# Optimization experiments

Hardware: AMD Instinct MI355X
Metric: run time of the kernel (lower is better)

## Reference

```python
import jax, jax.numpy as jnp
import numpy as np

B, D, H, DR, DM = 16384, 384, 1024, 512, 1152
KP, KN = 3, 2
K = KP + KN
RG_C = 8.0

def setup_inputs() -> dict:
    key = jax.random.key(0)
    ks = jax.random.split(key, 24)
    def n(k, shape, scale=1.0):
        return jax.random.normal(k, shape, jnp.float32) * scale
    s = lambda fan: 1.0 / np.sqrt(fan).astype(np.float32)
    return dict(
        init_f=n(ks[0], (B, D)),
        head_embs=n(ks[1], (K, B, D)),
        pred_embs=n(ks[2], (K, B, D)),
        w_ap=n(ks[3], (D, 1), s(D)), b_ap=jnp.zeros((1,), jnp.float32),
        w_an=n(ks[4], (D, 1), s(D)), b_an=jnp.zeros((1,), jnp.float32),
        nt_w1=n(ks[5], (D, H), s(D)), nt_b1=jnp.zeros((H,), jnp.float32),
        nt_w2=n(ks[6], (H, D), s(H)), nt_b2=jnp.zeros((D,), jnp.float32),
        g1=jnp.ones((D,), jnp.float32),
        rg_wx=n(ks[7], (D, DR), s(D)), rg_bx=jnp.zeros((DR,), jnp.float32),
        rg_wy=n(ks[8], (D, DR), s(D)), rg_by=jnp.zeros((DR,), jnp.float32),
        rg_wr=n(ks[9], (DR, DR), s(DR)), rg_br=jnp.zeros((DR,), jnp.float32),
        rg_wi=n(ks[10], (DR, DR), s(DR)), rg_bi=jnp.zeros((DR,), jnp.float32),
        rg_lam=n(ks[11], (DR,), 0.5),
        rg_wo=n(ks[12], (DR, D), s(DR)), rg_bo=jnp.zeros((D,), jnp.float32),
        g2=jnp.ones((D,), jnp.float32),
        mlp_wg=n(ks[13], (D, DM), s(D)),
        mlp_wv=n(ks[14], (D, DM), s(D)),
        mlp_wo=n(ks[15], (DM, D), s(DM)),
        fa_wg=n(ks[16], (D, D), s(D)),
        fa_wv=n(ks[17], (D, D), s(D)),
        fa_wo=n(ks[18], (D, D), s(D)),
        fa_wl=n(ks[19], (D, 1), s(D)), fa_bl=jnp.zeros((1,), jnp.float32),
    )

def rmsnorm(x, g, eps=1e-6):
    return x * g * jax.lax.rsqrt(jnp.mean(x * x, axis=-1, keepdims=True) + eps)

def rg_lru(x, wr, br, wi, bi, lam):
    # x: [B, S, DR] -> gated linear recurrence over S (Griffin RG-LRU)
    a_base = -RG_C * jax.nn.softplus(lam)  # [DR]
    def step(h, xt):
        r = jax.nn.sigmoid(xt @ wr + br)
        i = jax.nn.sigmoid(xt @ wi + bi)
        log_a = a_base * r
        h = jnp.exp(log_a) * h + jnp.sqrt(1.0 - jnp.exp(2.0 * log_a)) * (i * xt)
        return h, h
    h0 = jnp.zeros((x.shape[0], x.shape[2]), x.dtype)
    _, ys = jax.lax.scan(step, h0, jnp.swapaxes(x, 0, 1))
    return jnp.swapaxes(ys, 0, 1)

def reference(init_f, head_embs, pred_embs, w_ap, b_ap, w_an, b_an,
              nt_w1, nt_b1, nt_w2, nt_b2, g1,
              rg_wx, rg_bx, rg_wy, rg_by, rg_wr, rg_br, rg_wi, rg_bi,
              rg_lam, rg_wo, rg_bo, g2, mlp_wg, mlp_wv, mlp_wo,
              fa_wg, fa_wv, fa_wo, fa_wl, fa_bl):
    # message passing: estimate_tail_emb(head, pred) = head + pred (TransE-style)
    msg = head_embs + pred_embs                       # [K, B, D]
    pos = jnp.transpose(msg[:KP], (1, 0, 2))          # [B, KP, D]
    neg = jnp.transpose(msg[KP:], (1, 0, 2))          # [B, KN, D]
    # signed residual for negated atomics: -m + MLP(m)
    neg = -neg + jax.nn.relu(neg @ nt_w1 + nt_b1) @ nt_w2 + nt_b2
    # grouped softmax attention over the positive / negative message lists
    aw_p = jax.nn.softmax(pos @ w_ap + b_ap, axis=1)  # [B, KP, 1]
    aw_n = jax.nn.softmax(neg @ w_an + b_an, axis=1)  # [B, KN, 1]
    x = jnp.concatenate([init_f[:, None, :], pos * aw_p, neg * aw_n], axis=1)  # [B, S=6, D]
    # Griffin block (depth=1): recurrent residual branch
    h = rmsnorm(x, g1)
    u = h @ rg_wx + rg_bx                             # [B, S, DR]
    y = rg_lru(u, rg_wr, rg_br, rg_wi, rg_bi, rg_lam)
    gate = jax.nn.gelu(h @ rg_wy + rg_by)
    x = x + (y * gate) @ rg_wo + rg_bo
    # gated-MLP residual branch
    h2 = rmsnorm(x, g2)
    x = x + (jax.nn.gelu(h2 @ mlp_wg) * (h2 @ mlp_wv)) @ mlp_wo
    # final attention aggregation: Gated_MLP_block -> Linear(D,1) -> softmax -> mean
    fa = (jax.nn.gelu(x @ fa_wg) * (x @ fa_wv)) @ fa_wo
    w = jax.nn.softmax(fa @ fa_wl + fa_bl, axis=1)    # [B, S, 1]
    return jnp.mean(x * w, axis=1)                    # [B, D], agg_func='mean'
```

## Files before the change

kernel.cpp:

```cpp
#include <hip/hip_runtime.h>
#include <hip/hip_bf16.h>

#define B_TOT 16384
#define DD    384
#define HH    1024
#define DRR   512
#define DMM   1152
#define SS    6
#define KPP   3
#define KNN   2

typedef unsigned short ushort_t;
typedef __bf16 bf16x8 __attribute__((ext_vector_type(8)));
typedef float  f32x4  __attribute__((ext_vector_type(4)));

#define CST 136
#define EPW 72

__device__ __forceinline__ float fexp2(float x) { return __builtin_amdgcn_exp2f(x); }
__device__ __forceinline__ float frcp(float x)  { return __builtin_amdgcn_rcpf(x); }
__device__ __forceinline__ float sigmoid_f(float x) {
    return frcp(1.f + fexp2(-1.4426950408889634f * x));
}
__device__ __forceinline__ float gelu_f(float x) {
    float z = 0.7978845608028654f * x * (1.f + 0.044715f * x * x);
    return x * frcp(1.f + fexp2(-2.885390081777927f * z));
}
__device__ __forceinline__ float wave_red_sum(float v) {
    #pragma unroll
    for (int off = 32; off; off >>= 1) v += __shfl_xor(v, off);
    return v;
}
__device__ __forceinline__ ushort_t f2bf(float v) {
    __hip_bfloat16 h = __float2bfloat16(v);
    return *reinterpret_cast<ushort_t*>(&h);
}
__device__ __forceinline__ float bf2f(ushort_t u) {
    unsigned int x = ((unsigned int)u) << 16;
    return __uint_as_float(x);
}
__device__ __forceinline__ void g2l16(const ushort_t* g, ushort_t* l) {
    __builtin_amdgcn_global_load_lds(
        (const __attribute__((address_space(1))) void*)g,
        (__attribute__((address_space(3))) void*)l, 16, 0, 0);
}
__device__ __forceinline__ void swz_xy(int& bx, int& by) {
    const int nx = gridDim.x;
    const int nwg = nx * gridDim.y;
    const int h = by * nx + bx;
    const int q = nwg >> 3, r = nwg & 7;
    const int xcd = h & 7, lo = h >> 3;
    const int lin = (xcd < r) ? (xcd * (q + 1) + lo)
                              : (r * (q + 1) + (xcd - r) * q + lo);
    bx = lin % nx;
    by = lin / nx;
}

template<int EPI, bool ACCUM>
__global__ __launch_bounds__(256, 2)
void bgemm(const ushort_t* __restrict__ A, const ushort_t* __restrict__ WT,
           const float* __restrict__ bias, const ushort_t* __restrict__ X2,
           float* __restrict__ C, ushort_t* __restrict__ Ch, ushort_t* __restrict__ Ch2,
           int M, int N, int K)
{
    __shared__ ushort_t sm[32768];

    int bx = blockIdx.x, by = blockIdx.y;
    swz_xy(bx, by);
    const int tid = threadIdx.x;
    const int l = tid & 63, w = tid >> 6;
    const int wr = w >> 1, wc = w & 1;
    const int lr = l & 15, hi = l >> 4;
    const int row0 = by * 128, col0 = bx * 128;

    const int lrw = l >> 3;
    const int lch = (l & 7) ^ (lrw & 7);
    const ushort_t* As[4]; const ushort_t* Bs[4]; int lo_[4];
    #pragma unroll
    for (int i = 0; i < 4; ++i) {
        const int g = w * 4 + i;
        As[i] = A  + (size_t)(row0 + g*8 + lrw) * K + lch * 8;
        Bs[i] = WT + (size_t)(col0 + g*8 + lrw) * K + lch * 8;
        lo_[i] = g * 512;
    }
    const int ko[2] = {(hi*8) ^ ((lr&7)*8), (32 + hi*8) ^ ((lr&7)*8)};

    f32x4 acc[4][4] = {};
    const int NT = K >> 6;

    #pragma unroll
    for (int i = 0; i < 4; ++i) {
        g2l16(As[i], &sm[lo_[i]]);
        g2l16(Bs[i], &sm[16384 + lo_[i]]);
    }
    __syncthreads();

    int db = 0;
    for (int t = 0; t < NT; ++t) {
        if (t + 1 < NT) {
            const int nb = db ^ 1;
            #pragma unroll
            for (int i = 0; i < 4; ++i) {
                g2l16(As[i] + (size_t)(t+1)*64, &sm[nb*8192 + lo_[i]]);
                g2l16(Bs[i] + (size_t)(t+1)*64, &sm[16384 + nb*8192 + lo_[i]]);
            }
        }
        #pragma unroll
        for (int ks = 0; ks < 2; ++ks) {
            bf16x8 af[4], bfr[4];
            #pragma unroll
            for (int m = 0; m < 4; ++m)
                af[m] = *(const bf16x8*)&sm[db*8192 + (wr*64 + m*16 + lr)*64 + ko[ks]];
            #pragma unroll
            for (int n = 0; n < 4; ++n)
                bfr[n] = *(const bf16x8*)&sm[16384 + db*8192 + (wc*64 + n*16 + lr)*64 + ko[ks]];
            #pragma unroll
            for (int m = 0; m < 4; ++m)
                #pragma unroll
                for (int n = 0; n < 4; ++n)
                    acc[m][n] = __builtin_amdgcn_mfma_f32_16x16x32_bf16(
                        af[m], bfr[n], acc[m][n], 0, 0, 0);
        }
        __syncthreads();
        db ^= 1;
    }

    const bool BF = (EPI == 7) || (Ch != nullptr);
    #pragma unroll
    for (int m = 0; m < 4; ++m) {
        #pragma unroll
        for (int n = 0; n < 4; ++n) {
            const int r0 = row0 + wr*64 + m*16 + hi*4;
            const int c  = col0 + wc*64 + n*16 + lr;
            const float bv = bias ? bias[c] : 0.f;
            #pragma unroll
            for (int j = 0; j < 4; ++j) {
                const int r = r0 + j;
                float v = acc[m][n][j] + bv;
                if (EPI == 1) v = fmaxf(v, 0.f);
                if (EPI == 4) v = v - bf2f(X2[(size_t)r * N + c]);
                if (ACCUM)    v += C[(size_t)r * N + c];
                if (C) C[(size_t)r * N + c] = v;
                if (BF) {
                    float ov = (EPI == 7 && c >= 512) ? gelu_f(v) : v;
                    sm[(wr*64 + m*16 + hi*4 + j) * CST + wc*64 + n*16 + lr] = f2bf(ov);
                }
            }
        }
    }
    if (BF) {
        __syncthreads();
        const int er = tid >> 1, ec = (tid & 1) * 64;
        ushort_t* dst; int nn, dc0;
        if (EPI == 7) {
            nn = 512;
            if (col0 < 512) { dst = Ch;  dc0 = col0; }
            else            { dst = Ch2; dc0 = col0 - 512; }
        } else { dst = Ch; nn = N; dc0 = col0; }
        const uint4* sp = (const uint4*)&sm[er * CST + ec];
        uint4* gp = (uint4*)(dst + (size_t)(row0 + er) * nn + dc0 + ec);
        #pragma unroll
        for (int q = 0; q < 8; ++q) gp[q] = sp[q];
    }
}

template<bool LOGITS>
__global__ __launch_bounds__(256, 2)
void dual_k(const ushort_t* __restrict__ A, const ushort_t* __restrict__ W1T,
            const ushort_t* __restrict__ W2T, ushort_t* __restrict__ Ch,
            float* __restrict__ LP, const float* __restrict__ wproj,
            int M, int N, int K)
{
    __shared__ ushort_t sm[32768];

    int bx = blockIdx.x, by = blockIdx.y;
    swz_xy(bx, by);
    const int tid = threadIdx.x;
    const int l = tid & 63, w = tid >> 6;
    const int wr = w >> 1, wc = w & 1;
    const int lr = l & 15, hi = l >> 4;
    const int row0 = by * 128, col0 = bx * 64;

    const int lrw = l >> 3;
    const int lch = (l & 7) ^ (lrw & 7);
    const ushort_t* As[4]; int loA[4];
    #pragma unroll
    for (int i = 0; i < 4; ++i) {
        const int g = w * 4 + i;
        As[i] = A + (size_t)(row0 + g*8 + lrw) * K + lch * 8;
        loA[i] = g * 512;
    }
    const ushort_t* Gs[2]; const ushort_t* Vs[2]; int loB[2];
    #pragma unroll
    for (int i = 0; i < 2; ++i) {
        const int g = w * 2 + i;
        Gs[i] = W1T + (size_t)(col0 + g*8 + lrw) * K + lch * 8;
        Vs[i] = W2T + (size_t)(col0 + g*8 + lrw) * K + lch * 8;
        loB[i] = g * 512;
    }
    const int ko[2] = {(hi*8) ^ ((lr&7)*8), (32 + hi*8) ^ ((lr&7)*8)};

    f32x4 ag[4][2] = {}, av[4][2] = {};
    const int NT = K >> 6;

    #pragma unroll
    for (int i = 0; i < 4; ++i) g2l16(As[i], &sm[loA[i]]);
    #pragma unroll
    for (int i = 0; i < 2; ++i) {
        g2l16(Gs[i], &sm[16384 + loB[i]]);
        g2l16(Vs[i], &sm[24576 + loB[i]]);
    }
    __syncthreads();

    int db = 0;
    for (int t = 0; t < NT; ++t) {
        if (t + 1 < NT) {
            const int nb = db ^ 1;
            #pragma unroll
            for (int i = 0; i < 4; ++i)
                g2l16(As[i] + (size_t)(t+1)*64, &sm[nb*8192 + loA[i]]);
            #pragma unroll
            for (int i = 0; i < 2; ++i) {
                g2l16(Gs[i] + (size_t)(t+1)*64, &sm[16384 + nb*4096 + loB[i]]);
                g2l16(Vs[i] + (size_t)(t+1)*64, &sm[24576 + nb*4096 + loB[i]]);
            }
        }
        #pragma unroll
        for (int ks = 0; ks < 2; ++ks) {
            bf16x8 af[4], bg[2], bv[2];
            #pragma unroll
            for (int m = 0; m < 4; ++m)
                af[m] = *(const bf16x8*)&sm[db*8192 + (wr*64 + m*16 + lr)*64 + ko[ks]];
            #pragma unroll
            for (int n = 0; n < 2; ++n) {
                bg[n] = *(const bf16x8*)&sm[16384 + db*4096 + (wc*32 + n*16 + lr)*64 + ko[ks]];
                bv[n] = *(const bf16x8*)&sm[24576 + db*4096 + (wc*32 + n*16 + lr)*64 + ko[ks]];
            }
            #pragma unroll
            for (int m = 0; m < 4; ++m)
                #pragma unroll
                for (int n = 0; n < 2; ++n) {
                    ag[m][n] = __builtin_amdgcn_mfma_f32_16x16x32_bf16(af[m], bg[n], ag[m][n], 0, 0, 0);
                    av[m][n] = __builtin_amdgcn_mfma_f32_16x16x32_bf16(af[m], bv[n], av[m][n], 0, 0, 0);
                }
        }
        __syncthreads();
        db ^= 1;
    }

    if (!LOGITS) {
        #pragma unroll
        for (int m = 0; m < 4; ++m)
            #pragma unroll
            for (int n = 0; n < 2; ++n)
                #pragma unroll
                for (int j = 0; j < 4; ++j)
                    sm[(wr*64 + m*16 + hi*4 + j) * EPW + wc*32 + n*16 + lr] =
                        f2bf(gelu_f(ag[m][n][j]) * av[m][n][j]);
        __syncthreads();
        const int er = tid >> 1, ec = (tid & 1) * 32;
        const uint4* sp = (const uint4*)&sm[er * EPW + ec];
        uint4* gp = (uint4*)(Ch + (size_t)(row0 + er) * N + col0 + ec);
        #pragma unroll
        for (int q = 0; q < 4; ++q) gp[q] = sp[q];
    } else {
        float wp[2];
        #pragma unroll
        for (int n = 0; n < 2; ++n) wp[n] = wproj[col0 + wc*32 + n*16 + lr];
        float* red = (float*)sm;
        #pragma unroll
        for (int m = 0; m < 4; ++m) {
            #pragma unroll
            for (int j = 0; j < 4; ++j) {
                float s = 0.f;
                #pragma unroll
                for (int n = 0; n < 2; ++n)
                    s += gelu_f(ag[m][n][j]) * av[m][n][j] * wp[n];
                s += __shfl_xor(s, 1);
                s += __shfl_xor(s, 2);
                s += __shfl_xor(s, 4);
                s += __shfl_xor(s, 8);
                if (lr == 0) red[(wr*64 + m*16 + hi*4 + j) * 2 + wc] = s;
            }
        }
        __syncthreads();
        if (tid < 128)
            LP[(size_t)(row0 + tid) * 6 + bx] = red[tid*2] + red[tid*2 + 1];
    }
}

__global__ __launch_bounds__(256, 8)
void rec_k(ushort_t* __restrict__ u, const ushort_t* __restrict__ gate,
           const ushort_t* __restrict__ ri, const float* __restrict__ a2,
           int Bc)
{
    const int g = blockIdx.x * 256 + threadIdx.x;
    const int b = g >> 6, c8 = (g & 63) << 3;
    float a2v[8];
    *(float4*)&a2v[0] = *(const float4*)&a2[c8];
    *(float4*)&a2v[4] = *(const float4*)&a2[c8 + 4];
    float h[8] = {};
    for (int t = 0; t < SS; ++t) {
        const size_t row = (size_t)t * Bc + b;
        uint4 uw = *(const uint4*)&u[row * DRR + c8];
        uint4 rw = *(const uint4*)&ri[row * 1024 + c8];
        uint4 iw = *(const uint4*)&ri[row * 1024 + 512 + c8];
        uint4 gw = *(const uint4*)&gate[row * DRR + c8];
        const ushort_t* up = (const ushort_t*)&uw;
        const ushort_t* rp = (const ushort_t*)&rw;
        const ushort_t* ip = (const ushort_t*)&iw;
        const ushort_t* gp = (const ushort_t*)&gw;
        ushort_t o[8];
        #pragma unroll
        for (int q = 0; q < 8; ++q) {
            const float rv = sigmoid_f(bf2f(rp[q]));
            const float iv = sigmoid_f(bf2f(ip[q]));
            const float e  = fexp2(a2v[q] * rv);
            const float hv = e * h[q]
                           + sqrtf(fmaxf(0.f, 1.f - e * e)) * (iv * bf2f(up[q]));
            h[q] = hv;
            o[q] = f2bf(hv * bf2f(gp[q]));
        }
        *(uint4*)&u[row * DRR + c8] = *(const uint4*)o;
    }
}


struct TrArgs { const float* W[12]; };
__global__ void tr_all_k(TrArgs a, ushort_t* __restrict__ wt)
{
    constexpr int KT[12]  = {384,1024,384,384,512,512,512,384,384,1152,384,384};
    constexpr int NTb[12] = {1024,384,512,512,512,512,384,1152,1152,384,384,384};
    constexpr int EOFF[12]= {0,393216,786432,983040,1179648,1441792,1703936,
                             1900544,2342912,2785280,3227648,3375104};
    constexpr int TPRE[13]= {0,384,768,960,1152,1408,1664,1856,2288,2720,3152,3296,3440};
    const int tb = blockIdx.x;
    int s = 0;
    #pragma unroll
    for (int i = 0; i < 12; ++i) if (tb >= TPRE[i+1]) s = i + 1;
    const int rel = tb - TPRE[s];
    const int K = KT[s], N = NTb[s];
    const int ntn = N >> 5;
    const int k0 = (rel / ntn) * 32, n0 = (rel % ntn) * 32;

    __shared__ float ts[32][33];
    const int r = threadIdx.x >> 3, c4 = (threadIdx.x & 7) * 4;
    const float4 v = *(const float4*)&a.W[s][(size_t)(k0 + r) * N + n0 + c4];
    ts[r][c4+0] = v.x; ts[r][c4+1] = v.y; ts[r][c4+2] = v.z; ts[r][c4+3] = v.w;
    __syncthreads();
    ushort_t o4[4];
    #pragma unroll
    for (int q = 0; q < 4; ++q) o4[q] = f2bf(ts[c4 + q][r]);
    *(uint2*)&wt[EOFF[s] + (size_t)(n0 + r) * K + k0 + c4] = *(const uint2*)o4;
}

__global__ void prep_k(const float* __restrict__ rg_bx, const float* __restrict__ rg_by,
                       const float* __restrict__ rg_lam,
                       const float* __restrict__ rg_br, const float* __restrict__ rg_bi,
                       float* __restrict__ bias_xy, float* __restrict__ a2,
                       float* __restrict__ bias_ri)
{
    int i = blockIdx.x * 256 + threadIdx.x;
    if (i < 512) {
        bias_xy[i] = rg_bx[i];
        bias_ri[i] = rg_br[i];
        float lam = rg_lam[i];
        float sp = (lam > 20.f) ? lam : log1pf(expf(lam));
        a2[i] = -8.0f * sp * 1.4426950408889634f;
    } else if (i < 1024) {
        bias_xy[i] = rg_by[i - 512];
        bias_ri[i] = rg_bi[i - 512];
    }
}

__global__ void negm_k(const float* __restrict__ head, const float* __restrict__ pred,
                       ushort_t* __restrict__ negm_h, int b0, int Bc)
{
    int idx = blockIdx.x * 256 + threadIdx.x;
    int d = idx % DD, rr = idx / DD;
    int j = (rr >= Bc) ? 1 : 0;
    int b = rr - j * Bc;
    size_t off = ((size_t)(KPP + j) * B_TOT + (b0 + b)) * DD + d;
    negm_h[idx] = f2bf(head[off] + pred[off]);
}

__global__ void asmrms_k(const float* __restrict__ init_f,
                         const float* __restrict__ head, const float* __restrict__ pred,
                         const float* __restrict__ w_ap, const float* __restrict__ b_ap,
                         const float* __restrict__ w_an, const float* __restrict__ b_an,
                         const ushort_t* __restrict__ nf, const float* __restrict__ g1,
                         float* __restrict__ x, ushort_t* __restrict__ hb,
                         int b0, int Bc)
{
    const int lb = blockIdx.x, gb = b0 + lb, lane = threadIdx.x;
    float hp[3][6], nv[2][6], iv[6], wap[6], wan[6];
    #pragma unroll
    for (int q = 0; q < 6; ++q) {
        int d = lane + 64 * q;
        wap[q] = w_ap[d]; wan[q] = w_an[d];
        iv[q] = init_f[(size_t)gb * DD + d];
    }
    float lp[3], ln2[2];
    #pragma unroll
    for (int j = 0; j < 3; ++j) {
        float p = 0.f;
        #pragma unroll
        for (int q = 0; q < 6; ++q) {
            int d = lane + 64 * q;
            size_t off = ((size_t)j * B_TOT + gb) * DD + d;
            float v = head[off] + pred[off];
            hp[j][q] = v;
            p += v * wap[q];
        }
        lp[j] = wave_red_sum(p) + b_ap[0];
    }
    #pragma unroll
    for (int j = 0; j < 2; ++j) {
        float p = 0.f;
        #pragma unroll
        for (int q = 0; q < 6; ++q) {
            int d = lane + 64 * q;
            float v = bf2f(nf[((size_t)j * Bc + lb) * DD + d]);
            nv[j][q] = v;
            p += v * wan[q];
        }
        ln2[j] = wave_red_sum(p) + b_an[0];
    }
    float mp = fmaxf(lp[0], fmaxf(lp[1], lp[2]));
    float e0 = expf(lp[0]-mp), e1 = expf(lp[1]-mp), e2 = expf(lp[2]-mp);
    float sp = e0 + e1 + e2;
    float awp[3] = {e0/sp, e1/sp, e2/sp};
    float mn = fmaxf(ln2[0], ln2[1]);
    float f0 = expf(ln2[0]-mn), f1 = expf(ln2[1]-mn);
    float sn = f0 + f1;
    float awn[2] = {f0/sn, f1/sn};

    #pragma unroll
    for (int t = 0; t < SS; ++t) {
        float rowv[6], ss = 0.f;
        #pragma unroll
        for (int q = 0; q < 6; ++q) {
            float v;
            if (t == 0)      v = iv[q];
            else if (t <= 3) v = hp[t-1][q] * awp[t-1];
            else             v = nv[t-4][q] * awn[t-4];
            rowv[q] = v;
            ss += v * v;
        }
        ss = wave_red_sum(ss);
        float sc = rsqrtf(ss / (float)DD + 1e-6f);
        float* xr = x + (size_t)(t * Bc + lb) * DD;
        ushort_t* hr = hb + (size_t)(t * Bc + lb) * DD;
        #pragma unroll
        for (int q = 0; q < 6; ++q) {
            int d = lane + 64 * q;
            xr[d] = rowv[q];
            hr[d] = f2bf(rowv[q] * g1[d] * sc);
        }
    }
}

__global__ void rms_k(const float* __restrict__ x, const float* __restrict__ g,
                      ushort_t* __restrict__ h)
{
    int row  = blockIdx.x * 4 + (threadIdx.x >> 6);
    int lane = threadIdx.x & 63;
    const float* xr = x + (size_t)row * DD;
    float ss = 0.f;
    for (int d = lane; d < DD; d += 64) { float v = xr[d]; ss += v * v; }
    ss = wave_red_sum(ss);
    float sc = rsqrtf(ss / (float)DD + 1e-6f);
    ushort_t* hr = h + (size_t)row * DD;
    for (int d = lane; d < DD; d += 64) hr[d] = f2bf(xr[d] * g[d] * sc);
}

__global__ void wproj_k(const float* __restrict__ fa_wo, const float* __restrict__ fa_wl,
                        float* __restrict__ wproj)
{
    int d = threadIdx.x;
    float s = 0.f;
    for (int k = 0; k < DD; ++k) s += fa_wo[(size_t)d * DD + k] * fa_wl[k];
    wproj[d] = s;
}

__global__ void final_k(const float* __restrict__ x, const float* __restrict__ lp,
                        const float* __restrict__ fa_bl,
                        float* __restrict__ out, int b0, int Bc)
{
    const int lb = blockIdx.x, gb = b0 + lb, lane = threadIdx.x;
    float lg[SS];
    #pragma unroll
    for (int t = 0; t < SS; ++t) {
        const float* pp = lp + (size_t)(t * Bc + lb) * 6;
        lg[t] = pp[0] + pp[1] + pp[2] + pp[3] + pp[4] + pp[5] + fa_bl[0];
    }
    float m = lg[0];
    #pragma unroll
    for (int t = 1; t < SS; ++t) m = fmaxf(m, lg[t]);
    float e[SS], s = 0.f;
    #pragma unroll
    for (int t = 0; t < SS; ++t) { e[t] = expf(lg[t] - m); s += e[t]; }
    float inv = 1.0f / s;
    #pragma unroll
    for (int q = 0; q < 6; ++q) {
        int d = lane + 64 * q;
        float acc = 0.f;
        #pragma unroll
        for (int t = 0; t < SS; ++t)
            acc += x[(size_t)(t * Bc + lb) * DD + d] * (e[t] * inv);
        out[(size_t)gb * DD + d] = acc * (1.0f / 6.0f);
    }
}

extern "C" void kernel_launch(void* const* d_in, const int* in_sizes, int n_in,
                              void* d_out, int out_size, void* d_ws, size_t ws_size,
                              hipStream_t stream)
{
    (void)in_sizes; (void)n_in; (void)out_size;
    const float* init_f  = (const float*)d_in[0];
    const float* head    = (const float*)d_in[1];
    const float* pred    = (const float*)d_in[2];
    const float* w_ap    = (const float*)d_in[3];
    const float* b_ap    = (const float*)d_in[4];
    const float* w_an    = (const float*)d_in[5];
    const float* b_an    = (const float*)d_in[6];
    const float* nt_w1   = (const float*)d_in[7];
    const float* nt_b1   = (const float*)d_in[8];
    const float* nt_w2   = (const float*)d_in[9];
    const float* nt_b2   = (const float*)d_in[10];
    const float* g1      = (const float*)d_in[11];
    const float* rg_wx   = (const float*)d_in[12];
    const float* rg_bx   = (const float*)d_in[13];
    const float* rg_wy   = (const float*)d_in[14];
    const float* rg_by   = (const float*)d_in[15];
    const float* rg_wr   = (const float*)d_in[16];
    const float* rg_br   = (const float*)d_in[17];
    const float* rg_wi   = (const float*)d_in[18];
    const float* rg_bi   = (const float*)d_in[19];
    const float* rg_lam  = (const float*)d_in[20];
    const float* rg_wo   = (const float*)d_in[21];
    const float* rg_bo   = (const float*)d_in[22];
    const float* g2      = (const float*)d_in[23];
    const float* mlp_wg  = (const float*)d_in[24];
    const float* mlp_wv  = (const float*)d_in[25];
    const float* mlp_wo  = (const float*)d_in[26];
    const float* fa_wg   = (const float*)d_in[27];
    const float* fa_wv   = (const float*)d_in[28];
    const float* fa_wo   = (const float*)d_in[29];
    const float* fa_wl   = (const float*)d_in[30];
    const float* fa_bl   = (const float*)d_in[31];
    float* out = (float*)d_out;

    float* ws_f    = (float*)d_ws;
    float* wproj   = ws_f;
    float* bias_xy = ws_f + 512;
    float* a2      = ws_f + 1536;
    float* bias_ri = ws_f + 2048;
    ushort_t* wt   = (ushort_t*)(ws_f + 3072);

    ushort_t* ntw1T = wt + 0;
    ushort_t* ntw2T = wt + 393216;
    ushort_t* wxyT  = wt + 786432;
    ushort_t* wriT  = wt + 1179648;
    ushort_t* woT   = wt + 1703936;
    ushort_t* mwgT  = wt + 1900544;
    ushort_t* mwvT  = wt + 2342912;
    ushort_t* mwoT  = wt + 2785280;
    ushort_t* fwgT  = wt + 3227648;
    ushort_t* fwvT  = wt + 3375104;

    TrArgs ta;
    ta.W[0]=nt_w1; ta.W[1]=nt_w2; ta.W[2]=rg_wx; ta.W[3]=rg_wy;
    ta.W[4]=rg_wr; ta.W[5]=rg_wi; ta.W[6]=rg_wo; ta.W[7]=mlp_wg;
    ta.W[8]=mlp_wv; ta.W[9]=mlp_wo; ta.W[10]=fa_wg; ta.W[11]=fa_wv;
    tr_all_k<<<3440, 256, 0, stream>>>(ta, wt);
    prep_k<<<4, 256, 0, stream>>>(rg_bx, rg_by, rg_lam, rg_br, rg_bi,
                                  bias_xy, a2, bias_ri);
    wproj_k<<<1, DD, 0, stream>>>(fa_wo, fa_wl, wproj);

    const size_t fixed_f32 = 3072 + 1761280;
    const size_t per_b_f32 = 8448;
    int Bc = B_TOT;
    while (Bc > 128 && (fixed_f32 + per_b_f32 * (size_t)Bc) * 4 > ws_size) Bc >>= 1;

    float* arena = ws_f + fixed_f32;

    for (int b0 = 0; b0 < B_TOT; b0 += Bc) {
        const int M  = Bc * SS;
        const int M2 = Bc * KNN;
        float*    xbuf = arena;
        ushort_t* negm = (ushort_t*)(arena + (size_t)2304 * Bc);
        ushort_t* hid  = (ushort_t*)(arena + (size_t)2688 * Bc);
        ushort_t* nf   = (ushort_t*)(arena + (size_t)3712 * Bc);
        ushort_t* hb   = (ushort_t*)(arena + (size_t)4096 * Bc);
        ushort_t* uh   = (ushort_t*)(arena + (size_t)5376 * Bc);
        ushort_t* gth  = (ushort_t*)(arena + (size_t)6912 * Bc);
        ushort_t* ri   = (ushort_t*)(arena + (size_t)2304 * Bc);
        ushort_t* h2   = (ushort_t*)(arena + (size_t)2304 * Bc);
        ushort_t* Th   = (ushort_t*)(arena + (size_t)3456 * Bc);
        ushort_t* xh   = (ushort_t*)(arena + (size_t)6912 * Bc);
        float*    lpb  = arena + (size_t)2304 * Bc;

        negm_k<<<Bc * 3, 256, 0, stream>>>(head, pred, negm, b0, Bc);
        bgemm<1, false><<<dim3(HH/128, M2/128), 256, 0, stream>>>(
            negm, ntw1T, nt_b1, nullptr, nullptr, hid, nullptr, M2, HH, DD);
        bgemm<4, false><<<dim3(DD/128, M2/128), 256, 0, stream>>>(
            hid, ntw2T, nt_b2, negm, nullptr, nf, nullptr, M2, DD, HH);
        asmrms_k<<<Bc, 64, 0, stream>>>(init_f, head, pred, w_ap, b_ap, w_an, b_an,
                                        nf, g1, xbuf, hb, b0, Bc);

        bgemm<7, false><<<dim3(1024/128, M/128), 256, 0, stream>>>(
            hb, wxyT, bias_xy, nullptr, nullptr, uh, gth, M, 1024, DD);
        bgemm<0, false><<<dim3(1024/128, M/128), 256, 0, stream>>>(
            uh, wriT, bias_ri, nullptr, nullptr, ri, nullptr, M, 1024, DRR);
        rec_k<<<Bc / 4, 256, 0, stream>>>(uh, gth, ri, a2, Bc);
        bgemm<0, true><<<dim3(DD/128, M/128), 256, 0, stream>>>(
            uh, woT, rg_bo, nullptr, xbuf, nullptr, nullptr, M, DD, DRR);

        rms_k<<<M / 4, 256, 0, stream>>>(xbuf, g2, h2);
        dual_k<false><<<dim3(DMM/64, M/128), 256, 0, stream>>>(
            h2, mwgT, mwvT, Th, nullptr, nullptr, M, DMM, DD);
        bgemm<0, true><<<dim3(DD/128, M/128), 256, 0, stream>>>(
            Th, mwoT, nullptr, nullptr, xbuf, xh, nullptr, M, DD, DMM);

        dual_k<true><<<dim3(DD/64, M/128), 256, 0, stream>>>(
            xh, fwgT, fwvT, nullptr, lpb, wproj, M, DD, DD);
        final_k<<<Bc, 64, 0, stream>>>(xbuf, lpb, fa_bl, out, b0, Bc);
    }
}
```

Before: 1.659 ms.

## Deepen GEMM prefetch to two tiles ahead with explicit vmcnt waits

Both GEMM kernels now prefetch the K-tile two steps ahead into the buffer just consumed. Each step first loads all LDS fragments for the tile into registers, then barriers, then issues the global-to-LDS loads, then runs the MFMAs. Partial vmcnt waits replace full __syncthreads, so one tile's loads stay in flight while the current tile is computed. This is meant to hide global memory latency, at the cost of more live registers for the fragments and the risk of fragile hand-written waitcnt counts.

New measurement: 1.612 ms. 1.03x faster.

```diff
diff --git a/kernel.cpp b/kernel.cpp
--- a/kernel.cpp
+++ b/kernel.cpp
@@ -93,35 +93,49 @@
         g2l16(As[i], &sm[lo_[i]]);
         g2l16(Bs[i], &sm[16384 + lo_[i]]);
     }
-    __syncthreads();
+    #pragma unroll
+    for (int i = 0; i < 4; ++i) {
+        g2l16(As[i] + 64, &sm[8192 + lo_[i]]);
+        g2l16(Bs[i] + 64, &sm[16384 + 8192 + lo_[i]]);
+    }
+    asm volatile("s_waitcnt vmcnt(8)" ::: "memory");
+    __builtin_amdgcn_s_barrier();
 
     int db = 0;
     for (int t = 0; t < NT; ++t) {
-        if (t + 1 < NT) {
-            const int nb = db ^ 1;
+        bf16x8 af[2][4], bfr[2][4];
+        #pragma unroll
+        for (int ks = 0; ks < 2; ++ks) {
+            #pragma unroll
+            for (int m = 0; m < 4; ++m)
+                af[ks][m] = *(const bf16x8*)&sm[db*8192 + (wr*64 + m*16 + lr)*64 + ko[ks]];
+            #pragma unroll
+            for (int n = 0; n < 4; ++n)
+                bfr[ks][n] = *(const bf16x8*)&sm[16384 + db*8192 + (wc*64 + n*16 + lr)*64 + ko[ks]];
+        }
+        asm volatile("s_waitcnt lgkmcnt(0)" ::: "memory");
+        __builtin_amdgcn_sched_barrier(0);
+        __builtin_amdgcn_s_barrier();
+        if (t + 2 < NT) {
             #pragma unroll
             for (int i = 0; i < 4; ++i) {
-                g2l16(As[i] + (size_t)(t+1)*64, &sm[nb*8192 + lo_[i]]);
-                g2l16(Bs[i] + (size_t)(t+1)*64, &sm[16384 + nb*8192 + lo_[i]]);
+                g2l16(As[i] + (size_t)(t+2)*64, &sm[db*8192 + lo_[i]]);
+                g2l16(Bs[i] + (size_t)(t+2)*64, &sm[16384 + db*8192 + lo_[i]]);
             }
         }
         #pragma unroll
-        for (int ks = 0; ks < 2; ++ks) {
-            bf16x8 af[4], bfr[4];
-            #pragma unroll
-            for (int m = 0; m < 4; ++m)
-                af[m] = *(const bf16x8*)&sm[db*8192 + (wr*64 + m*16 + lr)*64 + ko[ks]];
-            #pragma unroll
-            for (int n = 0; n < 4; ++n)
-                bfr[n] = *(const bf16x8*)&sm[16384 + db*8192 + (wc*64 + n*16 + lr)*64 + ko[ks]];
+        for (int ks = 0; ks < 2; ++ks)
             #pragma unroll
             for (int m = 0; m < 4; ++m)
                 #pragma unroll
                 for (int n = 0; n < 4; ++n)
                     acc[m][n] = __builtin_amdgcn_mfma_f32_16x16x32_bf16(
-                        af[m], bfr[n], acc[m][n], 0, 0, 0);
-        }
-        __syncthreads();
+                        af[ks][m], bfr[ks][n], acc[m][n], 0, 0, 0);
+        if (t + 1 < NT) {
+            if (t + 2 < NT) asm volatile("s_waitcnt vmcnt(8)" ::: "memory");
+            else            asm volatile("s_waitcnt vmcnt(0)" ::: "memory");
+            __builtin_amdgcn_s_barrier();
+        }
         db ^= 1;
     }
 
@@ -210,41 +224,57 @@
         g2l16(Gs[i], &sm[16384 + loB[i]]);
         g2l16(Vs[i], &sm[24576 + loB[i]]);
     }
-    __syncthreads();
+    #pragma unroll
+    for (int i = 0; i < 4; ++i) g2l16(As[i] + 64, &sm[8192 + loA[i]]);
+    #pragma unroll
+    for (int i = 0; i < 2; ++i) {
+        g2l16(Gs[i] + 64, &sm[16384 + 4096 + loB[i]]);
+        g2l16(Vs[i] + 64, &sm[24576 + 4096 + loB[i]]);
+    }
+    asm volatile("s_waitcnt vmcnt(8)" ::: "memory");
+    __builtin_amdgcn_s_barrier();
 
     int db = 0;
     for (int t = 0; t < NT; ++t) {
-        if (t + 1 < NT) {
-            const int nb = db ^ 1;
+        bf16x8 af[2][4], bg[2][2], bv[2][2];
+        #pragma unroll
+        for (int ks = 0; ks < 2; ++ks) {
+            #pragma unroll
+            for (int m = 0; m < 4; ++m)
+                af[ks][m] = *(const bf16x8*)&sm[db*8192 + (wr*64 + m*16 + lr)*64 + ko[ks]];
+            #pragma unroll
+            for (int n = 0; n < 2; ++n) {
+                bg[ks][n] = *(const bf16x8*)&sm[16384 + db*4096 + (wc*32 + n*16 + lr)*64 + ko[ks]];
+                bv[ks][n] = *(const bf16x8*)&sm[24576 + db*4096 + (wc*32 + n*16 + lr)*64 + ko[ks]];
+            }
+        }
+        asm volatile("s_waitcnt lgkmcnt(0)" ::: "memory");
+        __builtin_amdgcn_sched_barrier(0);
+        __builtin_amdgcn_s_barrier();
+        if (t + 2 < NT) {
             #pragma unroll
             for (int i = 0; i < 4; ++i)
-                g2l16(As[i] + (size_t)(t+1)*64, &sm[nb*8192 + loA[i]]);
+                g2l16(As[i] + (size_t)(t+2)*64, &sm[db*8192 + loA[i]]);
             #pragma unroll
             for (int i = 0; i < 2; ++i) {
-                g2l16(Gs[i] + (size_t)(t+1)*64, &sm[16384 + nb*4096 + loB[i]]);
-                g2l16(Vs[i] + (size_t)(t+1)*64, &sm[24576 + nb*4096 + loB[i]]);
+                g2l16(Gs[i] + (size_t)(t+2)*64, &sm[16384 + db*4096 + loB[i]]);
+                g2l16(Vs[i] + (size_t)(t+2)*64, &sm[24576 + db*4096 + loB[i]]);
             }
         }
         #pragma unroll
-        for (int ks = 0; ks < 2; ++ks) {
-            bf16x8 af[4], bg[2], bv[2];
-            #pragma unroll
-            for (int m = 0; m < 4; ++m)
-                af[m] = *(const bf16x8*)&sm[db*8192 + (wr*64 + m*16 + lr)*64 + ko[ks]];
-            #pragma unroll
-            for (int n = 0; n < 2; ++n) {
-                bg[n] = *(const bf16x8*)&sm[16384 + db*4096 + (wc*32 + n*16 + lr)*64 + ko[ks]];
-                bv[n] = *(const bf16x8*)&sm[24576 + db*4096 + (wc*32 + n*16 + lr)*64 + ko[ks]];
-            }
+        for (int ks = 0; ks < 2; ++ks)
             #pragma unroll
             for (int m = 0; m < 4; ++m)
                 #pragma unroll
                 for (int n = 0; n < 2; ++n) {
-                    ag[m][n] = __builtin_amdgcn_mfma_f32_16x16x32_bf16(af[m], bg[n], ag[m][n], 0, 0, 0);
-                    av[m][n] = __builtin_amdgcn_mfma_f32_16x16x32_bf16(af[m], bv[n], av[m][n], 0, 0, 0);
+                    ag[m][n] = __builtin_amdgcn_mfma_f32_16x16x32_bf16(af[ks][m], bg[ks][n], ag[m][n], 0, 0, 0);
+                    av[m][n] = __builtin_amdgcn_mfma_f32_16x16x32_bf16(af[ks][m], bv[ks][n], av[m][n], 0, 0, 0);
                 }
-        }
-        __syncthreads();
+        if (t + 1 < NT) {
+            if (t + 2 < NT) asm volatile("s_waitcnt vmcnt(8)" ::: "memory");
+            else            asm volatile("s_waitcnt vmcnt(0)" ::: "memory");
+            __builtin_amdgcn_s_barrier();
+        }
         db ^= 1;
     }
 
```

## Single-buffer LDS in GEMM kernels to double occupancy, swizzle epilogue staging

Applied to the files above, without the earlier changes.

Both the bgemm and dual_k kernels drop LDS double buffering and cut shared memory from 64KB to 32KB per block, raising the launch bound from 2 to 4 blocks per CU. The next tile's global-to-LDS load is now issued after the compute barrier, so there is no intra-block overlap of load and MFMA. The design relies on more resident blocks to hide that latency instead. The epilogue staging moves from padded row strides to an XOR-swizzled layout so it fits in the smaller buffer. The risk is exposed load latency per block and register pressure from the higher occupancy bound, which could cause spills.

Result: faster. 1.468 ms (-11.5%).

```diff
diff --git a/kernel.cpp b/kernel.cpp
--- a/kernel.cpp
+++ b/kernel.cpp
@@ -13,9 +13,6 @@
 typedef unsigned short ushort_t;
 typedef __bf16 bf16x8 __attribute__((ext_vector_type(8)));
 typedef float  f32x4  __attribute__((ext_vector_type(4)));
-
-#define CST 136
-#define EPW 72
 
 __device__ __forceinline__ float fexp2(float x) { return __builtin_amdgcn_exp2f(x); }
 __device__ __forceinline__ float frcp(float x)  { return __builtin_amdgcn_rcpf(x); }
@@ -57,13 +54,13 @@
 }
 
 template<int EPI, bool ACCUM>
-__global__ __launch_bounds__(256, 2)
+__global__ __launch_bounds__(256, 4)
 void bgemm(const ushort_t* __restrict__ A, const ushort_t* __restrict__ WT,
            const float* __restrict__ bias, const ushort_t* __restrict__ X2,
            float* __restrict__ C, ushort_t* __restrict__ Ch, ushort_t* __restrict__ Ch2,
            int M, int N, int K)
 {
-    __shared__ ushort_t sm[32768];
+    __shared__ ushort_t sm[16384];
 
     int bx = blockIdx.x, by = blockIdx.y;
     swz_xy(bx, by);
@@ -91,29 +88,19 @@
     #pragma unroll
     for (int i = 0; i < 4; ++i) {
         g2l16(As[i], &sm[lo_[i]]);
-        g2l16(Bs[i], &sm[16384 + lo_[i]]);
-    }
-    __syncthreads();
-
-    int db = 0;
+        g2l16(Bs[i], &sm[8192 + lo_[i]]);
+    }
     for (int t = 0; t < NT; ++t) {
-        if (t + 1 < NT) {
-            const int nb = db ^ 1;
-            #pragma unroll
-            for (int i = 0; i < 4; ++i) {
-                g2l16(As[i] + (size_t)(t+1)*64, &sm[nb*8192 + lo_[i]]);
-                g2l16(Bs[i] + (size_t)(t+1)*64, &sm[16384 + nb*8192 + lo_[i]]);
-            }
-        }
+        __syncthreads();
         #pragma unroll
         for (int ks = 0; ks < 2; ++ks) {
             bf16x8 af[4], bfr[4];
             #pragma unroll
             for (int m = 0; m < 4; ++m)
-                af[m] = *(const bf16x8*)&sm[db*8192 + (wr*64 + m*16 + lr)*64 + ko[ks]];
+                af[m] = *(const bf16x8*)&sm[(wr*64 + m*16 + lr)*64 + ko[ks]];
             #pragma unroll
             for (int n = 0; n < 4; ++n)
-                bfr[n] = *(const bf16x8*)&sm[16384 + db*8192 + (wc*64 + n*16 + lr)*64 + ko[ks]];
+                bfr[n] = *(const bf16x8*)&sm[8192 + (wc*64 + n*16 + lr)*64 + ko[ks]];
             #pragma unroll
             for (int m = 0; m < 4; ++m)
                 #pragma unroll
@@ -122,7 +109,13 @@
                         af[m], bfr[n], acc[m][n], 0, 0, 0);
         }
         __syncthreads();
-        db ^= 1;
+        if (t + 1 < NT) {
+            #pragma unroll
+            for (int i = 0; i < 4; ++i) {
+                g2l16(As[i] + (size_t)(t+1)*64, &sm[lo_[i]]);
+                g2l16(Bs[i] + (size_t)(t+1)*64, &sm[8192 + lo_[i]]);
+            }
+        }
     }
 
     const bool BF = (EPI == 7) || (Ch != nullptr);
@@ -133,6 +126,8 @@
             const int r0 = row0 + wr*64 + m*16 + hi*4;
             const int c  = col0 + wc*64 + n*16 + lr;
             const float bv = bias ? bias[c] : 0.f;
+            const int rl0 = wr*64 + m*16 + hi*4;
+            const int cl  = wc*64 + n*16 + lr;
             #pragma unroll
             for (int j = 0; j < 4; ++j) {
                 const int r = r0 + j;
@@ -143,7 +138,8 @@
                 if (C) C[(size_t)r * N + c] = v;
                 if (BF) {
                     float ov = (EPI == 7 && c >= 512) ? gelu_f(v) : v;
-                    sm[(wr*64 + m*16 + hi*4 + j) * CST + wc*64 + n*16 + lr] = f2bf(ov);
+                    const int rl = rl0 + j;
+                    sm[rl*128 + ((((cl>>3) ^ (rl & 7))) << 3) + (cl & 7)] = f2bf(ov);
                 }
             }
         }
@@ -157,21 +153,24 @@
             if (col0 < 512) { dst = Ch;  dc0 = col0; }
             else            { dst = Ch2; dc0 = col0 - 512; }
         } else { dst = Ch; nn = N; dc0 = col0; }
-        const uint4* sp = (const uint4*)&sm[er * CST + ec];
-        uint4* gp = (uint4*)(dst + (size_t)(row0 + er) * nn + dc0 + ec);
-        #pragma unroll
-        for (int q = 0; q < 8; ++q) gp[q] = sp[q];
+        ushort_t* gp = dst + (size_t)(row0 + er) * nn + dc0 + ec;
+        #pragma unroll
+        for (int qq = 0; qq < 8; ++qq) {
+            const int q = (ec >> 3) + qq;
+            const uint4 vv = *(const uint4*)&sm[er*128 + ((q ^ (er & 7)) << 3)];
+            *(uint4*)(gp + qq*8) = vv;
+        }
     }
 }
 
 template<bool LOGITS>
-__global__ __launch_bounds__(256, 2)
+__global__ __launch_bounds__(256, 4)
 void dual_k(const ushort_t* __restrict__ A, const ushort_t* __restrict__ W1T,
             const ushort_t* __restrict__ W2T, ushort_t* __restrict__ Ch,
             float* __restrict__ LP, const float* __restrict__ wproj,
             int M, int N, int K)
 {
-    __shared__ ushort_t sm[32768];
+    __shared__ ushort_t sm[16384];
 
     int bx = blockIdx.x, by = blockIdx.y;
     swz_xy(bx, by);
@@ -207,34 +206,21 @@
     for (int i = 0; i < 4; ++i) g2l16(As[i], &sm[loA[i]]);
     #pragma unroll
     for (int i = 0; i < 2; ++i) {
-        g2l16(Gs[i], &sm[16384 + loB[i]]);
-        g2l16(Vs[i], &sm[24576 + loB[i]]);
-    }
-    __syncthreads();
-
-    int db = 0;
+        g2l16(Gs[i], &sm[8192  + loB[i]]);
+        g2l16(Vs[i], &sm[12288 + loB[i]]);
+    }
     for (int t = 0; t < NT; ++t) {
-        if (t + 1 < NT) {
-            const int nb = db ^ 1;
-            #pragma unroll
-            for (int i = 0; i < 4; ++i)
-                g2l16(As[i] + (size_t)(t+1)*64, &sm[nb*8192 + loA[i]]);
-            #pragma unroll
-            for (int i = 0; i < 2; ++i) {
-                g2l16(Gs[i] + (size_t)(t+1)*64, &sm[16384 + nb*4096 + loB[i]]);
-                g2l16(Vs[i] + (size_t)(t+1)*64, &sm[24576 + nb*4096 + loB[i]]);
-            }
-        }
+        __syncthreads();
         #pragma unroll
         for (int ks = 0; ks < 2; ++ks) {
             bf16x8 af[4], bg[2], bv[2];
             #pragma unroll
             for (int m = 0; m < 4; ++m)
-                af[m] = *(const bf16x8*)&sm[db*8192 + (wr*64 + m*16 + lr)*64 + ko[ks]];
+                af[m] = *(const bf16x8*)&sm[(wr*64 + m*16 + lr)*64 + ko[ks]];
             #pragma unroll
             for (int n = 0; n < 2; ++n) {
-                bg[n] = *(const bf16x8*)&sm[16384 + db*4096 + (wc*32 + n*16 + lr)*64 + ko[ks]];
-                bv[n] = *(const bf16x8*)&sm[24576 + db*4096 + (wc*32 + n*16 + lr)*64 + ko[ks]];
+                bg[n] = *(const bf16x8*)&sm[8192  + (wc*32 + n*16 + lr)*64 + ko[ks]];
+                bv[n] = *(const bf16x8*)&sm[12288 + (wc*32 + n*16 + lr)*64 + ko[ks]];
             }
             #pragma unroll
             for (int m = 0; m < 4; ++m)
@@ -245,24 +231,40 @@
                 }
         }
         __syncthreads();
-        db ^= 1;
+        if (t + 1 < NT) {
+            #pragma unroll
+            for (int i = 0; i < 4; ++i)
+                g2l16(As[i] + (size_t)(t+1)*64, &sm[loA[i]]);
+            #pragma unroll
+            for (int i = 0; i < 2; ++i) {
+                g2l16(Gs[i] + (size_t)(t+1)*64, &sm[8192  + loB[i]]);
+                g2l16(Vs[i] + (size_t)(t+1)*64, &sm[12288 + loB[i]]);
+            }
+        }
     }
 
     if (!LOGITS) {
         #pragma unroll
         for (int m = 0; m < 4; ++m)
             #pragma unroll
-            for (int n = 0; n < 2; ++n)
+            for (int n = 0; n < 2; ++n) {
+                const int cl = wc*32 + n*16 + lr;
                 #pragma unroll
-                for (int j = 0; j < 4; ++j)
-                    sm[(wr*64 + m*16 + hi*4 + j) * EPW + wc*32 + n*16 + lr] =
+                for (int j = 0; j < 4; ++j) {
+                    const int rl = wr*64 + m*16 + hi*4 + j;
+                    sm[rl*64 + (((cl>>3) ^ (rl & 7)) << 3) + (cl & 7)] =
                         f2bf(gelu_f(ag[m][n][j]) * av[m][n][j]);
+                }
+            }
         __syncthreads();
         const int er = tid >> 1, ec = (tid & 1) * 32;
-        const uint4* sp = (const uint4*)&sm[er * EPW + ec];
-        uint4* gp = (uint4*)(Ch + (size_t)(row0 + er) * N + col0 + ec);
-        #pragma unroll
-        for (int q = 0; q < 4; ++q) gp[q] = sp[q];
+        ushort_t* gp = Ch + (size_t)(row0 + er) * N + col0 + ec;
+        #pragma unroll
+        for (int qq = 0; qq < 4; ++qq) {
+            const int q = (ec >> 3) + qq;
+            const uint4 vv = *(const uint4*)&sm[er*64 + ((q ^ (er & 7)) << 3)];
+            *(uint4*)(gp + qq*8) = vv;
+        }
     } else {
         float wp[2];
         #pragma unroll
```
